# Kernel optimization log

Hardware: AMD Instinct MI355X
Metric: run time of the kernel (lower is better)

The kernel has to match this reference:

```python
import jax, jax.numpy as jnp
import numpy as np

N, C = 8192, 256
CQK = C // 8  # q/k projection dim = 32


def setup_inputs() -> dict:
    key = jax.random.key(0)
    k1, k2, k3, k4, k5 = jax.random.split(key, 5)
    f = jax.random.normal(k1, (N, C), dtype=jnp.float32)
    Wqk = jax.random.normal(k2, (CQK, C), dtype=jnp.float32) * (1.0 / np.sqrt(C))
    Wv = jax.random.normal(k3, (C, C), dtype=jnp.float32) * (1.0 / np.sqrt(C))
    bv = jax.random.normal(k4, (C,), dtype=jnp.float32) * 0.01
    gamma = jax.random.normal(k5, (1,), dtype=jnp.float32)
    return {"f": f, "Wqk": Wqk, "Wv": Wv, "bv": bv, "gamma": gamma}


def reference(f, Wqk, Wv, bv, gamma):
    # f: [N, C] point features. 1x1 convs over the point dim == per-point linear.
    q = f @ Wqk.T                      # [N, CQK] (q and k share weights)
    # energy[i, j] = <q_i, k_j>; q == k here, no 1/sqrt(d) scaling (faithful)
    energy = q @ q.T                   # [N, N]
    attn = jax.nn.softmax(energy, axis=-1)  # softmax over last dim (dim=-1)
    v = f @ Wv.T + bv                  # [N, C]
    # torch: bmm(x_v [1,C,N], attn [1,N,N]) -> out[c, j] = sum_i v[i, c] * attn[i, j]
    attn_out = jnp.einsum('ij,ic->jc', attn, v)  # [N, C]
    return gamma[0] * attn_out + f     # [N, C]
```

## Files before the change

kernel.cpp:

```cpp
#include <hip/hip_runtime.h>
#include <hip/hip_bf16.h>

#define NN 8192
#define CC 256
#define CQK 32
#define JS 4

using bf16x8 = __attribute__((ext_vector_type(8))) short;
using f16x8  = __attribute__((ext_vector_type(8))) _Float16;
using s16x4  = __attribute__((ext_vector_type(4))) short;
using f32x4  = __attribute__((ext_vector_type(4))) float;
using f32x16 = __attribute__((ext_vector_type(16))) float;

static __device__ __forceinline__ unsigned short f2bf(float x) {
    union { __hip_bfloat16 h; unsigned short u; } cv;
    cv.h = __float2bfloat16(x);
    return cv.u;
}
static __device__ __forceinline__ float bf2f(unsigned short u) {
    union { unsigned u; float f; } cv;
    cv.u = (unsigned)u << 16;
    return cv.f;
}
static __device__ __forceinline__ float fexp2(float x) { return __builtin_amdgcn_exp2f(x); }
static __device__ __forceinline__ int packbf(float lo, float hi) {
    union { float f; unsigned u; } a, b;
    a.f = lo; b.f = hi;
    return (int)((b.u & 0xFFFF0000u) | (a.u >> 16));
}

__global__ __launch_bounds__(256) void proj_q_kernel(
    const float* __restrict__ f, const float* __restrict__ Wqk,
    unsigned short* __restrict__ qf)
{
    __shared__ __align__(16) float fl[8][CC];
    const int t  = threadIdx.x;
    const int r0 = blockIdx.x * 8;
    {
        const float4* src = (const float4*)(f + (size_t)r0 * CC);
        float4* dst = (float4*)&fl[0][0];
        dst[t]       = src[t];
        dst[t + 256] = src[t + 256];
    }
    __syncthreads();
    const int cq = t & 31;
    const int rg = t >> 5;
    const float4* w4 = (const float4*)(Wqk + (size_t)cq * CC);
    float a = 0.f;
    for (int k4 = 0; k4 < 64; ++k4) {
        float4 wq = w4[k4];
        const float4 fv = *(const float4*)&fl[rg][k4 * 4];
        a = fmaf(wq.x, fv.x, a);
        a = fmaf(wq.y, fv.y, a);
        a = fmaf(wq.z, fv.z, a);
        a = fmaf(wq.w, fv.w, a);
    }
    a *= 1.2011224087864498f;
    union { _Float16 h; unsigned short u; } cv;
    cv.h = (_Float16)a;
    qf[(size_t)(r0 + rg) * CQK + cq] = cv.u;
}

__global__ __launch_bounds__(256, 4) void pass1v_kernel(
    const unsigned short* __restrict__ qf,
    const float* __restrict__ f, const float* __restrict__ Wv,
    const float* __restrict__ bv,
    float* __restrict__ ps, unsigned short* __restrict__ vB)
{
    __shared__ float rs[4][32];
    const int t    = threadIdx.x;
    const int lane = t & 63;
    const int w    = t >> 6;
    const int l31  = lane & 31;
    const int h    = lane >> 5;

    if (blockIdx.x < (NN / 32) * JS) {
        const int i0   = (blockIdx.x & 255) * 32;
        const int js   = blockIdx.x >> 8;
        const int JCH  = NN / JS / 4;
        const int jbase = js * (NN / JS) + w * JCH;

        const size_t qir = (size_t)(i0 + l31) * CQK;
        const f16x8 bi0 = *(const f16x8*)(qf + qir + 8 * h);
        const f16x8 bi1 = *(const f16x8*)(qf + qir + 16 + 8 * h);

        float s = 0.f;

#pragma unroll 2
        for (int st = 0; st < JCH; st += 32) {
            const size_t qjr = (size_t)(jbase + st + l31) * CQK;
            const f16x8 aj0 = *(const f16x8*)(qf + qjr + 8 * h);
            const f16x8 aj1 = *(const f16x8*)(qf + qjr + 16 + 8 * h);
            f32x16 ee = {0,0,0,0,0,0,0,0,0,0,0,0,0,0,0,0};
            ee = __builtin_amdgcn_mfma_f32_32x32x16_f16(aj0, bi0, ee, 0, 0, 0);
            ee = __builtin_amdgcn_mfma_f32_32x32x16_f16(aj1, bi1, ee, 0, 0, 0);
            float a_ = 0.f;
#pragma unroll
            for (int r = 0; r < 16; ++r) a_ += fexp2(ee[r]);
            s += a_;
        }
        s += __shfl_xor(s, 32);

        if (lane < 32) rs[w][l31] = s;
        __syncthreads();
        if (t < 32) {
            float sf = rs[0][t] + rs[1][t] + rs[2][t] + rs[3][t];
            ps[(size_t)js * NN + i0 + t] = sf;
        }
    } else {
        const int nb = (blockIdx.x - (NN / 32) * JS) * 32;
        const int cb = w * 64;

        f32x16 acc[2];
#pragma unroll
        for (int cf = 0; cf < 2; ++cf)
#pragma unroll
            for (int r = 0; r < 16; ++r) acc[cf][r] = 0.f;

        const float* frow = f + (size_t)(nb + l31) * CC;
#pragma unroll
        for (int ks = 0; ks < 16; ++ks) {
            const int k0 = ks * 16 + 8 * h;
            float4 a0 = *(const float4*)(frow + k0);
            float4 a1 = *(const float4*)(frow + k0 + 4);
            bf16x8 af;
            af[0] = (short)f2bf(a0.x); af[1] = (short)f2bf(a0.y);
            af[2] = (short)f2bf(a0.z); af[3] = (short)f2bf(a0.w);
            af[4] = (short)f2bf(a1.x); af[5] = (short)f2bf(a1.y);
            af[6] = (short)f2bf(a1.z); af[7] = (short)f2bf(a1.w);
#pragma unroll
            for (int cf = 0; cf < 2; ++cf) {
                const float* wrow = Wv + (size_t)(cb + 32 * cf + l31) * CC + k0;
                float4 b0 = *(const float4*)(wrow);
                float4 b1 = *(const float4*)(wrow + 4);
                bf16x8 bw;
                bw[0] = (short)f2bf(b0.x); bw[1] = (short)f2bf(b0.y);
                bw[2] = (short)f2bf(b0.z); bw[3] = (short)f2bf(b0.w);
                bw[4] = (short)f2bf(b1.x); bw[5] = (short)f2bf(b1.y);
                bw[6] = (short)f2bf(b1.z); bw[7] = (short)f2bf(b1.w);
                acc[cf] = __builtin_amdgcn_mfma_f32_32x32x16_bf16(af, bw, acc[cf], 0, 0, 0);
            }
        }
#pragma unroll
        for (int cf = 0; cf < 2; ++cf) {
            const int cg = cb + 32 * cf + l31;
            const float bvc = bv[cg];
#pragma unroll
            for (int rg = 0; rg < 4; ++rg) {
                const int ib = (nb >> 3) + rg;
                s16x4 pk;
#pragma unroll
                for (int r = 0; r < 4; ++r)
                    pk[r] = (short)f2bf(acc[cf][4 * rg + r] + bvc);
                *(s16x4*)(vB + ((size_t)ib * CC + cg) * 8 + 4 * h) = pk;
            }
        }
    }
}

__global__ __launch_bounds__(256) void finalize_kernel(
    const float* __restrict__ ps, float* __restrict__ bias)
{
    int i = blockIdx.x * 256 + threadIdx.x;
    float s = ps[i];
#pragma unroll
    for (int k = 1; k < JS; ++k) s += ps[(size_t)k * NN + i];
    bias[i] = __builtin_amdgcn_logf(s);
}

static __device__ __forceinline__ void swap2(int a_, int b_, int& lo, int& hi) {
#if __has_builtin(__builtin_amdgcn_permlane32_swap)
    auto r = __builtin_amdgcn_permlane32_swap(a_, b_, false, false);
    lo = r[0];
    hi = r[1];
#else
    const int h_ = (threadIdx.x & 63) >> 5;
    const int pa = __shfl_xor(a_, 32);
    const int pb = __shfl_xor(b_, 32);
    lo = h_ ? pb : a_;
    hi = h_ ? b_ : pa;
#endif
}

#define LOADQF(A0, A1, NI)                                                     \
    {                                                                          \
        const size_t qnr = (size_t)((NI) + l31) * CQK;                         \
        A0 = *(const f16x8*)(qf + qnr + 8 * h);                                \
        A1 = *(const f16x8*)(qf + qnr + 16 + 8 * h);                           \
    }

#define LOADVF2(VF, I)                                                         \
    _Pragma("unroll")                                                          \
    for (int s2 = 0; s2 < 2; ++s2)                                             \
        _Pragma("unroll")                                                      \
        for (int cf = 0; cf < 4; ++cf)                                         \
            VF[s2][cf] = *(const bf16x8*)(                                     \
                vB + ((size_t)(((I) >> 3) + 2 * s2 + h) * CC + cb + 32 * cf + l31) * 8);

#define LOADB42(B4, I)                                                         \
    _Pragma("unroll")                                                          \
    for (int rg = 0; rg < 4; ++rg)                                             \
        B4[rg] = *(const f32x4*)(bias + (I) + 8 * rg + 4 * h);

#define ECOMPF(EE, A0, A1)                                                     \
    {                                                                          \
        f32x16 z_ = {0,0,0,0,0,0,0,0,0,0,0,0,0,0,0,0};                         \
        z_ = __builtin_amdgcn_mfma_f32_32x32x16_f16(A1, bj1, z_, 0, 0, 0);     \
        EE = __builtin_amdgcn_mfma_f32_32x32x16_f16(A0, bj0, z_, 0, 0, 0);     \
    }

#define FINISH2(EE, B4, VF)                                                    \
    {                                                                          \
        int d0[4], d1[4];                                                      \
        _Pragma("unroll")                                                      \
        for (int rg = 0; rg < 4; ++rg) {                                       \
            float p0 = fexp2(EE[4 * rg + 0] - B4[rg][0]);                      \
            float p1 = fexp2(EE[4 * rg + 1] - B4[rg][1]);                      \
            float p2 = fexp2(EE[4 * rg + 2] - B4[rg][2]);                      \
            float p3 = fexp2(EE[4 * rg + 3] - B4[rg][3]);                      \
            d0[rg] = packbf(p0, p1);                                           \
            d1[rg] = packbf(p2, p3);                                           \
        }                                                                      \
        _Pragma("unroll")                                                      \
        for (int s2 = 0; s2 < 2; ++s2) {                                       \
            union { int i[4]; bf16x8 v; } pf;                                  \
            swap2(d0[2 * s2], d0[2 * s2 + 1], pf.i[0], pf.i[2]);               \
            swap2(d1[2 * s2], d1[2 * s2 + 1], pf.i[1], pf.i[3]);               \
            _Pragma("unroll")                                                  \
            for (int cf = 0; cf < 4; ++cf)                                     \
                acc[cf] = __builtin_amdgcn_mfma_f32_32x32x16_bf16(             \
                    pf.v, VF[s2][cf], acc[cf], 0, 0, 0);                       \
        }                                                                      \
    }

template<int ISPLIT, bool DIRECT>
__global__ __launch_bounds__(256, 2) void pass2_kernel(
    const unsigned short* __restrict__ qf,
    const unsigned short* __restrict__ vB,
    const float* __restrict__ bias,
    const float* __restrict__ f,
    const float* __restrict__ gp,
    void* __restrict__ dstv)
{
    const int t    = threadIdx.x;
    const int lane = t & 63;
    const int w    = t >> 6;
    const int l31  = lane & 31;
    const int h    = lane >> 5;
    const int bid  = blockIdx.x;

    int jblk, isp;
    if (ISPLIT == 4) {
        isp  = (bid & 7) >> 1;
        jblk = ((bid >> 3) << 1) | (bid & 1);
    } else if (ISPLIT == 2) {
        isp  = bid & 1;
        jblk = bid >> 1;
    } else {
        isp  = 0;
        jblk = bid;
    }
    const int jb   = jblk * 64;
    const int jrow = jb + 32 * (w & 1);
    const int cb   = 128 * (w >> 1);
    const int IL   = NN / ISPLIT;
    const int ibase = isp * IL;
    const int off  = ((bid ^ (bid >> 8)) & 1) * 32;

    const size_t qjr = (size_t)(jrow + l31) * CQK;
    const f16x8 bj0 = *(const f16x8*)(qf + qjr + 8 * h);
    const f16x8 bj1 = *(const f16x8*)(qf + qjr + 16 + 8 * h);

    f32x16 acc[4];
#pragma unroll
    for (int cf = 0; cf < 4; ++cf)
#pragma unroll
        for (int r = 0; r < 16; ++r) acc[cf][r] = 0.f;

    f32x16 eeA, eeB;
    f32x4  b4A[4], b4B[4];
    f16x8  qa0, qa1, qb0, qb1;
    bf16x8 vfA[2][4], vfB[2][4];

    const int m = IL - 1;
    const int iA0 = ibase + (off & m);
    const int iB0 = ibase + ((off + 32) & m);

    LOADQF(qa0, qa1, iA0)
    LOADB42(b4A, iA0)
    LOADVF2(vfA, iA0)
    ECOMPF(eeA, qa0, qa1)
    LOADQF(qb0, qb1, iB0)
    LOADB42(b4B, iB0)

    for (int k = 0; k < IL; k += 64) {
        const int iB = ibase + ((k + 32 + off) & m);
        const int n1 = ibase + ((k + 64 + off) & m);
        const int n2 = ibase + ((k + 96 + off) & m);
        LOADVF2(vfB, iB)
        ECOMPF(eeB, qb0, qb1)
        LOADQF(qa0, qa1, n1)
        FINISH2(eeA, b4A, vfA)
        LOADB42(b4A, n1)
        LOADVF2(vfA, n1)
        ECOMPF(eeA, qa0, qa1)
        LOADQF(qb0, qb1, n2)
        FINISH2(eeB, b4B, vfB)
        LOADB42(b4B, n2)
    }

    if (DIRECT) {
        float* dst = (float*)dstv;
        const float g = gp[0];
#pragma unroll
        for (int cf = 0; cf < 4; ++cf) {
            const int c = cb + 32 * cf + l31;
#pragma unroll
            for (int rg = 0; rg < 4; ++rg)
#pragma unroll
                for (int r = 0; r < 4; ++r) {
                    const int j = jrow + 4 * h + r + 8 * rg;
                    dst[(size_t)j * CC + c] =
                        fmaf(g, acc[cf][4 * rg + r], f[(size_t)j * CC + c]);
                }
        }
    } else {
        unsigned short* part = (unsigned short*)dstv + (size_t)isp * NN * CC;
#pragma unroll
        for (int cf = 0; cf < 4; ++cf) {
            const int c = cb + 32 * cf + l31;
#pragma unroll
            for (int rg = 0; rg < 4; ++rg)
#pragma unroll
                for (int r = 0; r < 4; ++r) {
                    const int j = jrow + 4 * h + r + 8 * rg;
                    part[(size_t)j * CC + c] = f2bf(acc[cf][4 * rg + r]);
                }
        }
    }
}

template<int SPLIT>
__global__ __launch_bounds__(256) void reduce_kernel(
    const unsigned short* __restrict__ part, const float* __restrict__ f,
    const float* __restrict__ gp, float* __restrict__ out)
{
    size_t idx = (size_t)blockIdx.x * 256 + threadIdx.x;
    float s0 = 0.f, s1 = 0.f, s2 = 0.f, s3 = 0.f;
#pragma unroll
    for (int k = 0; k < SPLIT; ++k) {
        const s16x4 v = *(const s16x4*)(part + (size_t)k * NN * CC + idx * 4);
        s0 += bf2f((unsigned short)v[0]);
        s1 += bf2f((unsigned short)v[1]);
        s2 += bf2f((unsigned short)v[2]);
        s3 += bf2f((unsigned short)v[3]);
    }
    const f32x4 fv = ((const f32x4*)f)[idx];
    const float g = gp[0];
    f32x4 o;
    o[0] = fmaf(g, s0, fv[0]);
    o[1] = fmaf(g, s1, fv[1]);
    o[2] = fmaf(g, s2, fv[2]);
    o[3] = fmaf(g, s3, fv[3]);
    ((f32x4*)out)[idx] = o;
}

extern "C" void kernel_launch(void* const* d_in, const int* in_sizes, int n_in,
                              void* d_out, int out_size, void* d_ws, size_t ws_size,
                              hipStream_t stream) {
    const float* f     = (const float*)d_in[0];
    const float* Wqk   = (const float*)d_in[1];
    const float* Wv    = (const float*)d_in[2];
    const float* bv    = (const float*)d_in[3];
    const float* gamma = (const float*)d_in[4];
    float* out = (float*)d_out;

    char* ws = (char*)d_ws;
    unsigned short* qf  = (unsigned short*)ws;
    unsigned short* vB  = (unsigned short*)(ws + (1 << 20));
    float* ps   = (float*)(ws + (5 << 20));
    float* bias = (float*)(ws + (5 << 20) + (256 << 10));
    unsigned short* part = (unsigned short*)(ws + (6 << 20));

    proj_q_kernel<<<dim3(NN / 8), dim3(256), 0, stream>>>(f, Wqk, qf);
    pass1v_kernel<<<dim3((NN / 32) * JS + NN / 32), dim3(256), 0, stream>>>(
        qf, f, Wv, bv, ps, vB);
    finalize_kernel<<<dim3(NN / 256), dim3(256), 0, stream>>>(ps, bias);

    const size_t PB = (size_t)NN * CC * 2;
    const size_t B0 = (size_t)6 << 20;
    if (ws_size >= B0 + 4 * PB) {
        pass2_kernel<4, false><<<dim3(128 * 4), dim3(256), 0, stream>>>(qf, vB, bias, f, gamma, part);
        reduce_kernel<4><<<dim3(NN * CC / 1024), dim3(256), 0, stream>>>(part, f, gamma, out);
    } else if (ws_size >= B0 + 2 * PB) {
        pass2_kernel<2, false><<<dim3(128 * 2), dim3(256), 0, stream>>>(qf, vB, bias, f, gamma, part);
        reduce_kernel<2><<<dim3(NN * CC / 1024), dim3(256), 0, stream>>>(part, f, gamma, out);
    } else {
        pass2_kernel<1, true><<<dim3(128), dim3(256), 0, stream>>>(qf, vB, bias, f, gamma, out);
    }
}
```

Baseline: 129.1 us.

## Fuse softmax-denominator finalize into pass2 via LDS and fold bias into MFMA init

Removes the separate finalize kernel launch. Each pass2 block now reduces the JS partial sums for its i-range, takes the log, and stores the result in shared memory. The negated bias is used as the MFMA accumulator initial value, so the per-element subtraction before exp2 disappears. This saves a launch and some VALU work, but every block redundantly recomputes the log-sum-exp of up to 2048–8192 entries and adds LDS usage that may affect occupancy.

```diff
diff --git a/kernel.cpp b/kernel.cpp
--- a/kernel.cpp
+++ b/kernel.cpp
@@ -158,16 +158,6 @@
     }
 }
 
-__global__ __launch_bounds__(256) void finalize_kernel(
-    const float* __restrict__ ps, float* __restrict__ bias)
-{
-    int i = blockIdx.x * 256 + threadIdx.x;
-    float s = ps[i];
-#pragma unroll
-    for (int k = 1; k < JS; ++k) s += ps[(size_t)k * NN + i];
-    bias[i] = __builtin_amdgcn_logf(s);
-}
-
 static __device__ __forceinline__ void swap2(int a_, int b_, int& lo, int& hi) {
 #if __has_builtin(__builtin_amdgcn_permlane32_swap)
     auto r = __builtin_amdgcn_permlane32_swap(a_, b_, false, false);
@@ -198,28 +188,31 @@
                 vB + ((size_t)(((I) >> 3) + 2 * s2 + h) * CC + cb + 32 * cf + l31) * 8);
 
 #define LOADB42(B4, I)                                                         \
-    _Pragma("unroll")                                                          \
-    for (int rg = 0; rg < 4; ++rg)                                             \
-        B4[rg] = *(const f32x4*)(bias + (I) + 8 * rg + 4 * h);
-
-#define ECOMPF(EE, A0, A1)                                                     \
     {                                                                          \
-        f32x16 z_ = {0,0,0,0,0,0,0,0,0,0,0,0,0,0,0,0};                         \
+        const int bo_ = (I) - ibase + 4 * h;                                   \
+        _Pragma("unroll")                                                      \
+        for (int rg = 0; rg < 4; ++rg)                                         \
+            B4[rg] = *(const f32x4*)&biasl[bo_ + 8 * rg];                      \
+    }
+
+#define ECOMPF(EE, A0, A1, B4)                                                 \
+    {                                                                          \
+        f32x16 z_;                                                             \
+        _Pragma("unroll")                                                      \
+        for (int rg = 0; rg < 4; ++rg)                                         \
+            _Pragma("unroll")                                                  \
+            for (int r = 0; r < 4; ++r) z_[4 * rg + r] = -B4[rg][r];           \
         z_ = __builtin_amdgcn_mfma_f32_32x32x16_f16(A1, bj1, z_, 0, 0, 0);     \
         EE = __builtin_amdgcn_mfma_f32_32x32x16_f16(A0, bj0, z_, 0, 0, 0);     \
     }
 
-#define FINISH2(EE, B4, VF)                                                    \
+#define FINISH2(EE, VF)                                                        \
     {                                                                          \
         int d0[4], d1[4];                                                      \
         _Pragma("unroll")                                                      \
         for (int rg = 0; rg < 4; ++rg) {                                       \
-            float p0 = fexp2(EE[4 * rg + 0] - B4[rg][0]);                      \
-            float p1 = fexp2(EE[4 * rg + 1] - B4[rg][1]);                      \
-            float p2 = fexp2(EE[4 * rg + 2] - B4[rg][2]);                      \
-            float p3 = fexp2(EE[4 * rg + 3] - B4[rg][3]);                      \
-            d0[rg] = packbf(p0, p1);                                           \
-            d1[rg] = packbf(p2, p3);                                           \
+            d0[rg] = packbf(fexp2(EE[4 * rg + 0]), fexp2(EE[4 * rg + 1]));     \
+            d1[rg] = packbf(fexp2(EE[4 * rg + 2]), fexp2(EE[4 * rg + 3]));     \
         }                                                                      \
         _Pragma("unroll")                                                      \
         for (int s2 = 0; s2 < 2; ++s2) {                                       \
@@ -237,11 +230,12 @@
 __global__ __launch_bounds__(256, 2) void pass2_kernel(
     const unsigned short* __restrict__ qf,
     const unsigned short* __restrict__ vB,
-    const float* __restrict__ bias,
+    const float* __restrict__ ps,
     const float* __restrict__ f,
     const float* __restrict__ gp,
     void* __restrict__ dstv)
 {
+    __shared__ float biasl[NN / ISPLIT];
     const int t    = threadIdx.x;
     const int lane = t & 63;
     const int w    = t >> 6;
@@ -267,6 +261,14 @@
     const int ibase = isp * IL;
     const int off  = ((bid ^ (bid >> 8)) & 1) * 32;
 
+    for (int idx = t; idx < IL; idx += 256) {
+        float s = ps[ibase + idx];
+#pragma unroll
+        for (int k = 1; k < JS; ++k) s += ps[(size_t)k * NN + ibase + idx];
+        biasl[idx] = __builtin_amdgcn_logf(s);
+    }
+    __syncthreads();
+
     const size_t qjr = (size_t)(jrow + l31) * CQK;
     const f16x8 bj0 = *(const f16x8*)(qf + qjr + 8 * h);
     const f16x8 bj1 = *(const f16x8*)(qf + qjr + 16 + 8 * h);
@@ -289,7 +291,7 @@
     LOADQF(qa0, qa1, iA0)
     LOADB42(b4A, iA0)
     LOADVF2(vfA, iA0)
-    ECOMPF(eeA, qa0, qa1)
+    ECOMPF(eeA, qa0, qa1, b4A)
     LOADQF(qb0, qb1, iB0)
     LOADB42(b4B, iB0)
 
@@ -298,14 +300,14 @@
         const int n1 = ibase + ((k + 64 + off) & m);
         const int n2 = ibase + ((k + 96 + off) & m);
         LOADVF2(vfB, iB)
-        ECOMPF(eeB, qb0, qb1)
+        ECOMPF(eeB, qb0, qb1, b4B)
         LOADQF(qa0, qa1, n1)
-        FINISH2(eeA, b4A, vfA)
+        FINISH2(eeA, vfA)
         LOADB42(b4A, n1)
         LOADVF2(vfA, n1)
-        ECOMPF(eeA, qa0, qa1)
+        ECOMPF(eeA, qa0, qa1, b4A)
         LOADQF(qb0, qb1, n2)
-        FINISH2(eeB, b4B, vfB)
+        FINISH2(eeB, vfB)
         LOADB42(b4B, n2)
     }
 
@@ -379,23 +381,21 @@
     unsigned short* qf  = (unsigned short*)ws;
     unsigned short* vB  = (unsigned short*)(ws + (1 << 20));
     float* ps   = (float*)(ws + (5 << 20));
-    float* bias = (float*)(ws + (5 << 20) + (256 << 10));
     unsigned short* part = (unsigned short*)(ws + (6 << 20));
 
     proj_q_kernel<<<dim3(NN / 8), dim3(256), 0, stream>>>(f, Wqk, qf);
     pass1v_kernel<<<dim3((NN / 32) * JS + NN / 32), dim3(256), 0, stream>>>(
         qf, f, Wv, bv, ps, vB);
-    finalize_kernel<<<dim3(NN / 256), dim3(256), 0, stream>>>(ps, bias);
 
     const size_t PB = (size_t)NN * CC * 2;
     const size_t B0 = (size_t)6 << 20;
     if (ws_size >= B0 + 4 * PB) {
-        pass2_kernel<4, false><<<dim3(128 * 4), dim3(256), 0, stream>>>(qf, vB, bias, f, gamma, part);
+        pass2_kernel<4, false><<<dim3(128 * 4), dim3(256), 0, stream>>>(qf, vB, ps, f, gamma, part);
         reduce_kernel<4><<<dim3(NN * CC / 1024), dim3(256), 0, stream>>>(part, f, gamma, out);
     } else if (ws_size >= B0 + 2 * PB) {
-        pass2_kernel<2, false><<<dim3(128 * 2), dim3(256), 0, stream>>>(qf, vB, bias, f, gamma, part);
+        pass2_kernel<2, false><<<dim3(128 * 2), dim3(256), 0, stream>>>(qf, vB, ps, f, gamma, part);
         reduce_kernel<2><<<dim3(NN * CC / 1024), dim3(256), 0, stream>>>(part, f, gamma, out);
     } else {
-        pass2_kernel<1, true><<<dim3(128), dim3(256), 0, stream>>>(qf, vB, bias, f, gamma, out);
-    }
-}
+        pass2_kernel<1, true><<<dim3(128), dim3(256), 0, stream>>>(qf, vB, ps, f, gamma, out);
+    }
+}
```

New measurement: 189.6 us. 1.47x slower.
